# Kernel tuning notes

Measured on AMD Instinct MI355X. Metric: run time of the kernel, lower is better.

## Reference

```python
import jax, jax.numpy as jnp
import numpy as np
from jax import lax

EMB, HID, L, PATCH, IMG, K = 192, 64, 6, 4, 224, 8
FMAP = IMG // PATCH
N = FMAP * FMAP
B = 8
ALG = 4
GB_np = np.array([0, 1, 1, 2])  # grade of each blade [1, e1, e2, e12]
GB = jnp.asarray(GB_np)

def _cayley_np():
    C = np.zeros((4, 4, 4), np.float32)
    tbl = {(0,0):(0,1.),(0,1):(1,1.),(0,2):(2,1.),(0,3):(3,1.),
           (1,0):(1,1.),(1,1):(0,1.),(1,2):(3,1.),(1,3):(2,1.),
           (2,0):(2,1.),(2,1):(3,-1.),(2,2):(0,1.),(2,3):(1,-1.),
           (3,0):(3,1.),(3,1):(2,-1.),(3,2):(1,1.),(3,3):(0,-1.)}
    for (i, j), (k, s) in tbl.items():
        C[i, j, k] = s
    return C

CAY_np = _cayley_np()
CAYLEY = jnp.asarray(CAY_np)
_paths = np.zeros((3, 3, 3), bool)
for _i in range(4):
    for _j in range(4):
        for _k in range(4):
            if CAY_np[_i, _j, _k] != 0:
                _paths[GB_np[_i], GB_np[_j], GB_np[_k]] = True
PI, PJ, PK = (jnp.asarray(a) for a in np.nonzero(_paths))
NPATH = int(_paths.sum())  # 10 geometric-product paths for Cl(2,0)

def build_knn_graph(H, W, k):
    yy, xx = np.meshgrid(np.arange(H, dtype=np.float32), np.arange(W, dtype=np.float32), indexing='ij')
    coords = np.stack([xx.ravel(), yy.ravel()], -1)
    cn = coords / np.array([W - 1, H - 1], np.float32) * 2 - 1
    d = np.linalg.norm(cn[:, None] - cn[None], axis=-1)
    np.fill_diagonal(d, np.inf)
    idx = np.argsort(d, axis=-1, kind='stable')[:, :k]
    rows = np.repeat(np.arange(H * W), k)
    cols = idx.reshape(-1)
    return rows.astype(np.int32), cols.astype(np.int32), cn.astype(np.float32)

def mvlin(x, W, b=None):
    # per-grade MVLinear: W [out,in,3] expanded to blades via GB
    y = jnp.einsum('nmi,bmi->bni', W[:, :, GB], x)
    if b is not None:
        y = y.at[:, :, 0].add(b)  # bias embedded in scalar blade only
    return y

def mvlin_flat(x, W, b):
    # subspaces=False MVLinear: same weight across blades
    y = jnp.einsum('nm,bmi->bni', W, x)
    return y.at[:, :, 0].add(b)

def mv_silu(x, a, b):
    # invariants: [scalar, q(grade1), q(grade2)]; gate = sigmoid(a*inv+b)
    inv = jnp.concatenate([x[..., :1], x[..., 1:2]**2 + x[..., 2:3]**2, x[..., 3:4]**2], -1)
    return jax.nn.sigmoid(a * inv + b)[..., GB] * x

def normalize_mv(x, a):
    q = jnp.concatenate([x[..., :1]**2, x[..., 1:2]**2 + x[..., 2:3]**2, x[..., 3:4]**2], -1)
    n = jnp.sqrt(q + 1e-12)
    d = jax.nn.sigmoid(a) * (n - 1.0) + 1.0
    return x / (d + 1e-6)[..., GB]

def sgp(x, Wl, bl, Wr, na, gw):
    # SteerableGeometricProductLayer
    xr = normalize_mv(mvlin(x, Wr), na)
    full = jnp.zeros((gw.shape[0], 3, 3, 3), x.dtype).at[:, PI, PJ, PK].set(gw)
    fb = full[:, GB][:, :, GB][:, :, :, GB]  # [feat,4,4,4]
    gp = jnp.einsum('bni,nijk,bnk->bnj', x, CAYLEY[None] * fb, xr)
    return (mvlin(x, Wl, bl) + gp) * np.float32(1.0 / np.sqrt(2.0))

def _forward(x, conv_w, conv_b, stem_g, stem_b, pos_embed, in_W, in_b, in_Wl, in_bl, in_Wr, in_na, in_gw, eg_eW, eg_eb, eg_sa, eg_sb, eg_nW, eg_nb, eg_Wl, eg_bl, eg_Wr, eg_na, eg_gw, eg_aa, eg_ab, out_W, out_b, on_g, on_b, cls_W, cls_b, coords, rows, cols):
    Bx = x.shape[0]
    # stem: strided conv + LayerNorm over (C,H,W)
    y = lax.conv_general_dilated(x, conv_w, (PATCH, PATCH), 'VALID', dimension_numbers=('NCHW', 'OIHW', 'NCHW')) + conv_b[None, :, None, None]
    mu = y.mean(axis=(1, 2, 3), keepdims=True)
    var = ((y - mu) ** 2).mean(axis=(1, 2, 3), keepdims=True)
    y = (y - mu) / jnp.sqrt(var + 1e-5) * stem_g[None] + stem_b[None]
    y = y + pos_embed
    feat = y.transpose(0, 2, 3, 1).reshape(Bx * N, EMB)
    # embed features in scalar blade, coordinates in vector blades e1,e2
    h = jnp.zeros((Bx * N, EMB + 1, ALG), x.dtype)
    h = h.at[:, :EMB, 0].set(feat)
    h = h.at[:, EMB, 1:3].set(jnp.tile(coords, (Bx, 1)))
    h = sgp(mvlin_flat(h, in_W, in_b), in_Wl, in_bl, in_Wr, in_na, in_gw)
    BN = Bx * N
    for i in range(L):
        m = mv_silu(mvlin(h[rows] - h[cols], eg_eW[i], eg_eb[i]), eg_sa[i], eg_sb[i])
        agg = jax.ops.segment_sum(m, rows, num_segments=BN)  # count computed but unused in original
        nu = mvlin(jnp.concatenate([h, agg], axis=1), eg_nW[i], eg_nb[i])
        out = mv_silu(sgp(nu, eg_Wl[i], eg_bl[i], eg_Wr[i], eg_na[i], eg_gw[i]), eg_aa[i], eg_ab[i])
        h = h + out if i > 0 else out
    s = mvlin_flat(h, out_W, out_b)[..., 0]
    mu2 = s.mean(-1, keepdims=True)
    v2 = ((s - mu2) ** 2).mean(-1, keepdims=True)
    s = (s - mu2) / jnp.sqrt(v2 + 1e-5) * on_g + on_b
    pooled = s.reshape(Bx, N, EMB).mean(axis=1)
    return pooled @ cls_W.T + cls_b

def setup_inputs() -> dict:
    key = jax.random.key(0)
    ks = iter(jax.random.split(key, 64))
    nrm = lambda shape, s=0.05: jax.random.normal(next(ks), shape, jnp.float32) * s
    rows, cols, cn = build_knn_graph(FMAP, FMAP, K)
    offs = np.arange(B, dtype=np.int32)[:, None] * N
    rows_b = (rows[None] + offs).reshape(-1)
    cols_b = (cols[None] + offs).reshape(-1)
    return dict(
        x=jax.random.normal(next(ks), (B, 3, IMG, IMG), jnp.float32),
        conv_w=nrm((EMB, 3, PATCH, PATCH)),
        conv_b=jnp.zeros((EMB,), jnp.float32),
        stem_g=jnp.ones((EMB, FMAP, FMAP), jnp.float32),
        stem_b=jnp.zeros((EMB, FMAP, FMAP), jnp.float32),
        pos_embed=nrm((1, EMB, FMAP, FMAP), 0.02),
        coords=jnp.asarray(cn),
        in_W=nrm((HID, EMB + 1)), in_b=jnp.zeros((HID,), jnp.float32),
        in_Wl=nrm((HID, HID, 3)), in_bl=jnp.zeros((HID,), jnp.float32),
        in_Wr=nrm((HID, HID, 3)), in_na=jnp.zeros((HID, 3), jnp.float32),
        in_gw=nrm((HID, NPATH), 0.2),
        eg_eW=nrm((L, HID, HID, 3)), eg_eb=jnp.zeros((L, HID), jnp.float32),
        eg_sa=jnp.ones((L, HID, 3), jnp.float32), eg_sb=jnp.zeros((L, HID, 3), jnp.float32),
        eg_nW=nrm((L, HID, 2 * HID, 3)), eg_nb=jnp.zeros((L, HID), jnp.float32),
        eg_Wl=nrm((L, HID, HID, 3)), eg_bl=jnp.zeros((L, HID), jnp.float32),
        eg_Wr=nrm((L, HID, HID, 3)), eg_na=jnp.zeros((L, HID, 3), jnp.float32),
        eg_gw=nrm((L, HID, NPATH), 0.2),
        eg_aa=jnp.ones((L, HID, 3), jnp.float32), eg_ab=jnp.zeros((L, HID, 3), jnp.float32),
        out_W=nrm((EMB, HID)), out_b=jnp.zeros((EMB,), jnp.float32),
        on_g=jnp.ones((EMB,), jnp.float32), on_b=jnp.zeros((EMB,), jnp.float32),
        cls_W=nrm((10, EMB), 0.02), cls_b=jnp.zeros((10,), jnp.float32),
        rows=jnp.asarray(rows_b), cols=jnp.asarray(cols_b),
    )

def reference(x, conv_w, conv_b, stem_g, stem_b, pos_embed, coords, in_W, in_b, in_Wl, in_bl, in_Wr, in_na, in_gw, eg_eW, eg_eb, eg_sa, eg_sb, eg_nW, eg_nb, eg_Wl, eg_bl, eg_Wr, eg_na, eg_gw, eg_aa, eg_ab, out_W, out_b, on_g, on_b, cls_W, cls_b, rows, cols):
    return _forward(x, conv_w, conv_b, stem_g, stem_b, pos_embed, in_W, in_b, in_Wl, in_bl, in_Wr, in_na, in_gw, eg_eW, eg_eb, eg_sa, eg_sb, eg_nW, eg_nb, eg_Wl, eg_bl, eg_Wr, eg_na, eg_gw, eg_aa, eg_ab, out_W, out_b, on_g, on_b, cls_W, cls_b, coords, rows, cols)
```

## Files before the change

kernel.cpp:

```cpp
#include <hip/hip_runtime.h>
#include <hip/hip_bf16.h>
#include <math.h>

#define EMBC   192
#define NLAY   6
#define IMGC   224
#define FMAPC  56
#define NNODE  3136
#define NBATCH 8
#define BNODES 25088
#define KNNE   8
#define NT     64
#define RSQRT2 0.70710678118654752f

__device__ __forceinline__ float sigm(float x){ return 1.0f/(1.0f+__expf(-x)); }

__device__ __forceinline__ void stage_tile(float* xs, const float* __restrict__ g,
                                           int p0, int tid){
  for(int t = tid; t < NT*256; t += 256){
    int n = t >> 8, q = t & 255;
    int m = q >> 2, bi = q & 3;
    xs[(n<<8) + (((m + n) & 63)<<2) + bi] = g[((size_t)(p0+n)<<8) + q];
  }
}

__global__ void k_tr(const float* __restrict__ g, const float* __restrict__ sb,
                     const float* __restrict__ pe, float* __restrict__ g2,
                     float* __restrict__ pb2){
  int n = blockIdx.x; int c = threadIdx.x;
  g2[n*EMBC + c]  = g[c*NNODE + n];
  pb2[n*EMBC + c] = sb[c*NNODE + n] + pe[c*NNODE + n];
}

__global__ __launch_bounds__(256) void k_conv(const float* __restrict__ x,
    const float* __restrict__ cw, const float* __restrict__ cb,
    float* __restrict__ y0, float* __restrict__ parts){
  __shared__ float xs[2688];
  __shared__ float wsh[9216];
  __shared__ float red[512];
  int blk = blockIdx.x; int b = blk / FMAPC; int ph = blk % FMAPC;
  int tid = threadIdx.x;
  for(int t = tid; t < 9216; t += 256) wsh[t] = cw[t];
  for(int t = tid; t < 2688; t += 256){
    int r = t / IMGC; int w = t % IMGC;
    int ci = r >> 2, kh = r & 3;
    xs[t] = x[((size_t)(b*3 + ci)*IMGC + (ph*4 + kh))*IMGC + w];
  }
  __syncthreads();
  float s1 = 0.f, s2 = 0.f;
  for(int oi = tid; oi < FMAPC*EMBC; oi += 256){
    int pw = oi / EMBC; int c = oi % EMBC;
    float acc = cb[c];
    const float4* wv4 = (const float4*)(wsh + c*48);
    #pragma unroll
    for(int r = 0; r < 12; ++r){
      float4 xv = *((const float4*)(xs + r*IMGC + pw*4));
      float4 wv = wv4[r];
      acc += xv.x*wv.x + xv.y*wv.y + xv.z*wv.z + xv.w*wv.w;
    }
    y0[((size_t)(b*NNODE + ph*FMAPC + pw))*EMBC + c] = acc;
    s1 += acc; s2 += acc*acc;
  }
  red[tid] = s1; red[256+tid] = s2;
  __syncthreads();
  for(int st = 128; st > 0; st >>= 1){
    if(tid < st){ red[tid] += red[tid+st]; red[256+tid] += red[256+tid+st]; }
    __syncthreads();
  }
  if(tid == 0){ parts[blk*2] = red[0]; parts[blk*2+1] = red[256]; }
}

__global__ void k_stats(const float* __restrict__ parts, float* __restrict__ stats){
  int b = threadIdx.x;
  if(b < NBATCH){
    float S = 0.f, Q = 0.f;
    for(int j = 0; j < FMAPC; ++j){ S += parts[(b*FMAPC+j)*2]; Q += parts[(b*FMAPC+j)*2+1]; }
    float cnt = (float)(EMBC*NNODE);
    float mu = S/cnt;
    float var = Q/cnt - mu*mu;
    stats[b*2] = mu; stats[b*2+1] = rsqrtf(var + 1e-5f);
  }
}

__global__ __launch_bounds__(256,2) void k_embed(const float* __restrict__ y0,
    const float* __restrict__ stats, const float* __restrict__ g2,
    const float* __restrict__ pb2, const float* __restrict__ inW,
    const float* __restrict__ inb, const float* __restrict__ coords,
    float* __restrict__ xmv){
  __shared__ float fs[NT*193];
  int tid = threadIdx.x, lane = tid & 63;
  int wid = __builtin_amdgcn_readfirstlane(tid >> 6);
  int ch0 = wid << 4;
  int p0 = blockIdx.x * NT;
  int b = p0 / NNODE; int n0 = p0 - b*NNODE;
  float mu = stats[b*2], rstd = stats[b*2+1];
  for(int t = tid; t < NT*192; t += 256){
    int n = t / 192, c = t - n*192;
    int nn = n0 + n;
    fs[n*193 + c] = (y0[(size_t)(p0+n)*192 + c] - mu)*rstd*g2[nn*192+c] + pb2[nn*192+c];
  }
  __syncthreads();
  float acc[16];
  #pragma unroll
  for(int ci = 0; ci < 16; ++ci) acc[ci] = 0.f;
  for(int m = 0; m < 192; ++m){
    float xm = fs[lane*193 + m];
    #pragma unroll
    for(int ci = 0; ci < 16; ++ci)
      acc[ci] += inW[(size_t)(ch0+ci)*193 + m] * xm;
  }
  float cx = coords[(n0+lane)*2], cy = coords[(n0+lane)*2+1];
  #pragma unroll
  for(int ci = 0; ci < 16; ++ci){
    int ch = ch0 + ci;
    float wc = inW[(size_t)ch*193 + 192];
    float4 v; v.x = acc[ci] + inb[ch]; v.y = wc*cx; v.z = wc*cy; v.w = 0.f;
    *((float4*)(xmv + ((size_t)(p0+lane)*64 + ch)*4)) = v;
  }
}

__global__ __launch_bounds__(256) void k_edge(const float* __restrict__ z,
    const int* __restrict__ cols, const float* __restrict__ eb,
    const float* __restrict__ sa, const float* __restrict__ sb,
    float* __restrict__ agg){
  int tid = threadIdx.x;
  int ch = tid & 63;
  int p = blockIdx.x*4 + (tid >> 6);
  float4 zo = *((const float4*)(z + ((size_t)p*64 + ch)*4));
  float bias = eb[ch];
  float a0 = sa[ch*3], a1 = sa[ch*3+1], a2 = sa[ch*3+2];
  float b0 = sb[ch*3], b1 = sb[ch*3+1], b2 = sb[ch*3+2];
  float ax=0.f, ay=0.f, az=0.f, aw=0.f;
  #pragma unroll
  for(int k = 0; k < KNNE; ++k){
    int c = cols[p*KNNE + k];
    float4 zc = *((const float4*)(z + ((size_t)c*64 + ch)*4));
    float d0 = zo.x - zc.x + bias;
    float d1 = zo.y - zc.y;
    float d2 = zo.z - zc.z;
    float d3 = zo.w - zc.w;
    float g0 = sigm(a0*d0 + b0);
    float g1 = sigm(a1*(d1*d1 + d2*d2) + b1);
    float g2v = sigm(a2*(d3*d3) + b2);
    ax += g0*d0; ay += g1*d1; az += g1*d2; aw += g2v*d3;
  }
  float4 acc; acc.x=ax; acc.y=ay; acc.z=az; acc.w=aw;
  *((float4*)(agg + ((size_t)p*64 + ch)*4)) = acc;
}

__global__ __launch_bounds__(256,2) void k_nu(const float* __restrict__ h,
    const float* __restrict__ agg, float* __restrict__ nu,
    const float* __restrict__ W, const float* __restrict__ nb){
  __shared__ float xs[NT*256];
  int tid = threadIdx.x, lane = tid & 63;
  int wid = __builtin_amdgcn_readfirstlane(tid >> 6);
  int ch0 = wid << 4;
  int p0 = blockIdx.x * NT;
  float acc[16][4];
  #pragma unroll
  for(int ci = 0; ci < 16; ++ci)
    #pragma unroll
    for(int bi = 0; bi < 4; ++bi) acc[ci][bi] = 0.f;
  const float* xbase = xs + (lane<<8);

  stage_tile(xs, h, p0, tid);
  __syncthreads();
  #pragma unroll 1
  for(int m = 0; m < 64; ++m){
    float4 xv = *((const float4*)(xbase + (((m + lane)&63)<<2)));
    #pragma unroll
    for(int ci = 0; ci < 16; ++ci){
      const float* wp = W + ((size_t)(ch0+ci)*128 + m)*3;
      float w0 = wp[0], w1 = wp[1], w2 = wp[2];
      acc[ci][0] += w0*xv.x; acc[ci][1] += w1*xv.y;
      acc[ci][2] += w1*xv.z; acc[ci][3] += w2*xv.w;
    }
  }
  __syncthreads();
  stage_tile(xs, agg, p0, tid);
  __syncthreads();
  #pragma unroll 1
  for(int m = 0; m < 64; ++m){
    float4 xv = *((const float4*)(xbase + (((m + lane)&63)<<2)));
    #pragma unroll
    for(int ci = 0; ci < 16; ++ci){
      const float* wp = W + ((size_t)(ch0+ci)*128 + 64 + m)*3;
      float w0 = wp[0], w1 = wp[1], w2 = wp[2];
      acc[ci][0] += w0*xv.x; acc[ci][1] += w1*xv.y;
      acc[ci][2] += w1*xv.z; acc[ci][3] += w2*xv.w;
    }
  }
  int p = p0 + lane;
  #pragma unroll
  for(int ci = 0; ci < 16; ++ci){
    int ch = ch0 + ci;
    float4 v; v.x = acc[ci][0] + nb[ch]; v.y = acc[ci][1];
    v.z = acc[ci][2]; v.w = acc[ci][3];
    *((float4*)(nu + ((size_t)p*64 + ch)*4)) = v;
  }
}

__global__ __launch_bounds__(256,2) void k_sgp(const float* __restrict__ src,
    float* __restrict__ h, const float* __restrict__ Wl, const float* __restrict__ bl,
    const float* __restrict__ Wr, const float* __restrict__ na,
    const float* __restrict__ gw, const float* __restrict__ aa,
    const float* __restrict__ ab, int mode,
    const float* __restrict__ zW, float* __restrict__ zout){
  __shared__ float xs[NT*256];
  int tid = threadIdx.x, lane = tid & 63;
  int wid = __builtin_amdgcn_readfirstlane(tid >> 6);
  int ch0 = wid << 4;
  int p0 = blockIdx.x * NT;
  stage_tile(xs, src, p0, tid);
  __syncthreads();
  float accl[16][4], accr[16][4];
  #pragma unroll
  for(int ci = 0; ci < 16; ++ci)
    #pragma unroll
    for(int bi = 0; bi < 4; ++bi){ accl[ci][bi] = 0.f; accr[ci][bi] = 0.f; }
  const float* xbase = xs + (lane<<8);
  #pragma unroll 1
  for(int m = 0; m < 64; ++m){
    float4 xv = *((const float4*)(xbase + (((m + lane)&63)<<2)));
    #pragma unroll
    for(int ci = 0; ci < 16; ++ci){
      const float* wlp = Wl + ((size_t)(ch0+ci)*64 + m)*3;
      const float* wrp = Wr + ((size_t)(ch0+ci)*64 + m)*3;
      float wl0 = wlp[0], wl1 = wlp[1], wl2 = wlp[2];
      float wr0 = wrp[0], wr1 = wrp[1], wr2 = wrp[2];
      accl[ci][0] += wl0*xv.x; accl[ci][1] += wl1*xv.y;
      accl[ci][2] += wl1*xv.z; accl[ci][3] += wl2*xv.w;
      accr[ci][0] += wr0*xv.x; accr[ci][1] += wr1*xv.y;
      accr[ci][2] += wr1*xv.z; accr[ci][3] += wr2*xv.w;
    }
  }
  float vout[16][4];
  int p = p0 + lane;
  #pragma unroll
  for(int ci = 0; ci < 16; ++ci){
    int ch = ch0 + ci;
    float yr0 = accr[ci][0], yr1 = accr[ci][1], yr2 = accr[ci][2], yr3 = accr[ci][3];
    float na0 = sigm(na[ch*3]), na1 = sigm(na[ch*3+1]), na2 = sigm(na[ch*3+2]);
    float d0 = na0*(sqrtf(yr0*yr0 + 1e-12f) - 1.f) + 1.f + 1e-6f;
    float d1 = na1*(sqrtf(yr1*yr1 + yr2*yr2 + 1e-12f) - 1.f) + 1.f + 1e-6f;
    float d2 = na2*(sqrtf(yr3*yr3 + 1e-12f) - 1.f) + 1.f + 1e-6f;
    float xr0 = yr0/d0, xr1 = yr1/d1, xr2 = yr2/d1, xr3 = yr3/d2;
    float4 xv = *((const float4*)(xbase + (((ch + lane)&63)<<2)));
    const float* gwp = gw + ch*10;
    float gp0 = gwp[0]*xv.x*xr0 + gwp[3]*(xv.y*xr1 + xv.z*xr2) + gwp[7]*xv.w*xr3;
    float gp1 = gwp[1]*xv.x*xr1 + gwp[4]*xv.y*xr0 - gwp[5]*xv.z*xr3 - gwp[8]*xv.w*xr2;
    float gp2 = gwp[1]*xv.x*xr2 + gwp[4]*xv.z*xr0 + gwp[5]*xv.y*xr3 + gwp[8]*xv.w*xr1;
    float gp3 = gwp[2]*xv.x*xr3 + gwp[6]*(xv.y*xr2 - xv.z*xr1) - gwp[9]*xv.w*xr0;
    float o0 = (accl[ci][0] + bl[ch] + gp0)*RSQRT2;
    float o1 = (accl[ci][1] + gp1)*RSQRT2;
    float o2 = (accl[ci][2] + gp2)*RSQRT2;
    float o3 = (accl[ci][3] + gp3)*RSQRT2;
    float v0, v1, v2, v3;
    if(mode == 0){ v0 = o0; v1 = o1; v2 = o2; v3 = o3; }
    else{
      float g0 = sigm(aa[ch*3]*o0 + ab[ch*3]);
      float g1 = sigm(aa[ch*3+1]*(o1*o1 + o2*o2) + ab[ch*3+1]);
      float g2v = sigm(aa[ch*3+2]*(o3*o3) + ab[ch*3+2]);
      v0 = g0*o0; v1 = g1*o1; v2 = g1*o2; v3 = g2v*o3;
      if(mode == 2){
        float4 hp = *((const float4*)(h + ((size_t)p*64 + ch)*4));
        v0 += hp.x; v1 += hp.y; v2 += hp.z; v3 += hp.w;
      }
    }
    float4 vv; vv.x=v0; vv.y=v1; vv.z=v2; vv.w=v3;
    *((float4*)(h + ((size_t)p*64 + ch)*4)) = vv;
    vout[ci][0]=v0; vout[ci][1]=v1; vout[ci][2]=v2; vout[ci][3]=v3;
  }
  if(zW != nullptr){
    __syncthreads();
    #pragma unroll
    for(int ci = 0; ci < 16; ++ci){
      int ch = ch0 + ci;
      float4 vv; vv.x=vout[ci][0]; vv.y=vout[ci][1]; vv.z=vout[ci][2]; vv.w=vout[ci][3];
      *((float4*)(xs + (lane<<8) + (((ch + lane)&63)<<2))) = vv;
    }
    __syncthreads();
    float accz[16][4];
    #pragma unroll
    for(int ci = 0; ci < 16; ++ci)
      #pragma unroll
      for(int bi = 0; bi < 4; ++bi) accz[ci][bi] = 0.f;
    #pragma unroll 1
    for(int m = 0; m < 64; ++m){
      float4 xv = *((const float4*)(xbase + (((m + lane)&63)<<2)));
      #pragma unroll
      for(int ci = 0; ci < 16; ++ci){
        const float* wp = zW + ((size_t)(ch0+ci)*64 + m)*3;
        float w0 = wp[0], w1 = wp[1], w2 = wp[2];
        accz[ci][0] += w0*xv.x; accz[ci][1] += w1*xv.y;
        accz[ci][2] += w1*xv.z; accz[ci][3] += w2*xv.w;
      }
    }
    #pragma unroll
    for(int ci = 0; ci < 16; ++ci){
      int ch = ch0 + ci;
      float4 v; v.x=accz[ci][0]; v.y=accz[ci][1]; v.z=accz[ci][2]; v.w=accz[ci][3];
      *((float4*)(zout + ((size_t)p*64 + ch)*4)) = v;
    }
  }
}

__global__ __launch_bounds__(256,2) void k_head(const float* __restrict__ h,
    const float* __restrict__ oW, const float* __restrict__ ob,
    const float* __restrict__ ong, const float* __restrict__ onb,
    float* __restrict__ s){
  __shared__ float hs[NT*65];
  __shared__ float rr[512];
  int tid = threadIdx.x, lane = tid & 63;
  int wid = __builtin_amdgcn_readfirstlane(tid >> 6);
  int c0 = wid*48;
  int p0 = blockIdx.x * NT;
  for(int t = tid; t < NT*64; t += 256){
    int n = t >> 6, c = t & 63;
    hs[n*65 + c] = h[(((size_t)(p0+n))*64 + c)*4];
  }
  __syncthreads();
  float a[48];
  #pragma unroll
  for(int ci = 0; ci < 48; ++ci) a[ci] = 0.f;
  #pragma unroll 1
  for(int m = 0; m < 64; ++m){
    float xm = hs[lane*65 + m];
    #pragma unroll
    for(int ci = 0; ci < 48; ++ci)
      a[ci] += oW[(size_t)(c0+ci)*64 + m] * xm;
  }
  float s1 = 0.f, s2 = 0.f;
  #pragma unroll
  for(int ci = 0; ci < 48; ++ci){
    a[ci] += ob[c0+ci];
    s1 += a[ci]; s2 += a[ci]*a[ci];
  }
  rr[wid*64 + lane] = s1; rr[256 + wid*64 + lane] = s2;
  __syncthreads();
  float S = rr[lane] + rr[64+lane] + rr[128+lane] + rr[192+lane];
  float Q = rr[256+lane] + rr[320+lane] + rr[384+lane] + rr[448+lane];
  float mu = S*(1.0f/EMBC);
  float var = Q*(1.0f/EMBC) - mu*mu;
  float rstd = rsqrtf(var + 1e-5f);
  #pragma unroll
  for(int q = 0; q < 12; ++q){
    int c = c0 + q*4;
    float4 v;
    v.x = (a[q*4  ] - mu)*rstd*ong[c  ] + onb[c  ];
    v.y = (a[q*4+1] - mu)*rstd*ong[c+1] + onb[c+1];
    v.z = (a[q*4+2] - mu)*rstd*ong[c+2] + onb[c+2];
    v.w = (a[q*4+3] - mu)*rstd*ong[c+3] + onb[c+3];
    *((float4*)(s + (size_t)(p0+lane)*192 + c)) = v;
  }
}

__global__ void k_pool1(const float* __restrict__ s, float* __restrict__ pp){
  int blk = blockIdx.x;
  int b = blk >> 5, chunk = blk & 31;
  int c = threadIdx.x;
  float acc = 0.f;
  int n0 = chunk*98;
  for(int j = 0; j < 98; ++j) acc += s[((size_t)(b*NNODE + n0 + j))*EMBC + c];
  pp[(size_t)blk*EMBC + c] = acc;
}
__global__ void k_pool2(const float* __restrict__ pp, float* __restrict__ pooled){
  int b = blockIdx.x; int c = threadIdx.x;
  float acc = 0.f;
  for(int j = 0; j < 32; ++j) acc += pp[((size_t)(b*32 + j))*EMBC + c];
  pooled[b*EMBC + c] = acc * (1.0f/NNODE);
}

__global__ void k_cls(const float* __restrict__ pooled, const float* __restrict__ cW,
                      const float* __restrict__ cb, float* __restrict__ out){
  int tid = threadIdx.x;
  if(tid < NBATCH*10){
    int b = tid/10, k = tid%10;
    float acc = cb[k];
    for(int c = 0; c < EMBC; ++c) acc += pooled[b*EMBC + c]*cW[k*EMBC + c];
    out[tid] = acc;
  }
}

extern "C" void kernel_launch(void* const* d_in, const int* in_sizes, int n_in,
                              void* d_out, int out_size, void* d_ws, size_t ws_size,
                              hipStream_t stream){
  const float* x      = (const float*)d_in[0];
  const float* conv_w = (const float*)d_in[1];
  const float* conv_b = (const float*)d_in[2];
  const float* stem_g = (const float*)d_in[3];
  const float* stem_b = (const float*)d_in[4];
  const float* pos_e  = (const float*)d_in[5];
  const float* coords = (const float*)d_in[6];
  const float* inW    = (const float*)d_in[7];
  const float* inb    = (const float*)d_in[8];
  const float* inWl   = (const float*)d_in[9];
  const float* inbl   = (const float*)d_in[10];
  const float* inWr   = (const float*)d_in[11];
  const float* inna   = (const float*)d_in[12];
  const float* ingw   = (const float*)d_in[13];
  const float* eg_eW  = (const float*)d_in[14];
  const float* eg_eb  = (const float*)d_in[15];
  const float* eg_sa  = (const float*)d_in[16];
  const float* eg_sb  = (const float*)d_in[17];
  const float* eg_nW  = (const float*)d_in[18];
  const float* eg_nb  = (const float*)d_in[19];
  const float* eg_Wl  = (const float*)d_in[20];
  const float* eg_bl  = (const float*)d_in[21];
  const float* eg_Wr  = (const float*)d_in[22];
  const float* eg_na  = (const float*)d_in[23];
  const float* eg_gw  = (const float*)d_in[24];
  const float* eg_aa  = (const float*)d_in[25];
  const float* eg_ab  = (const float*)d_in[26];
  const float* outW   = (const float*)d_in[27];
  const float* outb   = (const float*)d_in[28];
  const float* ong    = (const float*)d_in[29];
  const float* onb    = (const float*)d_in[30];
  const float* clsW   = (const float*)d_in[31];
  const float* clsb   = (const float*)d_in[32];
  const int*   cols   = (const int*)d_in[34];

  float* ws = (float*)d_ws;
  size_t off = 0;
  float* hbuf  = ws + off; off += (size_t)BNODES*256;
  float* bigA  = ws + off; off += (size_t)BNODES*256;
  float* bigB  = ws + off; off += (size_t)BNODES*256;
  float* g2    = ws + off; off += (size_t)NNODE*EMBC;
  float* pb2   = ws + off; off += (size_t)NNODE*EMBC;
  float* y0    = ws + off; off += (size_t)BNODES*EMBC;
  float* parts = ws + off; off += 896;
  float* stats = ws + off; off += 16;
  float* pp    = ws + off; off += 256*EMBC;
  float* pooled= ws + off; off += NBATCH*EMBC;

  const int NTILE = BNODES/NT;

  k_tr   <<<NNODE, 192, 0, stream>>>(stem_g, stem_b, pos_e, g2, pb2);
  k_conv <<<NBATCH*FMAPC, 256, 0, stream>>>(x, conv_w, conv_b, y0, parts);
  k_stats<<<1, 64, 0, stream>>>(parts, stats);
  k_embed<<<NTILE, 256, 0, stream>>>(y0, stats, g2, pb2, inW, inb, coords, bigA);
  k_sgp  <<<NTILE, 256, 0, stream>>>(bigA, hbuf, inWl, inbl, inWr, inna, ingw,
                                     (const float*)nullptr, (const float*)nullptr, 0,
                                     eg_eW, bigB);
  float* zcur = bigB;
  float* spare = bigA;
  for(int l = 0; l < NLAY; ++l){
    k_edge <<<BNODES/4, 256, 0, stream>>>(zcur, cols, eg_eb + l*64,
                                          eg_sa + l*192, eg_sb + l*192, spare);
    k_nu   <<<NTILE, 256, 0, stream>>>(hbuf, spare, zcur,
                                       eg_nW + (size_t)l*24576, eg_nb + l*64);
    const float* zWn = (l < NLAY-1) ? (eg_eW + (size_t)(l+1)*12288) : (const float*)nullptr;
    k_sgp  <<<NTILE, 256, 0, stream>>>(zcur, hbuf, eg_Wl + (size_t)l*12288, eg_bl + l*64,
                                       eg_Wr + (size_t)l*12288, eg_na + l*192,
                                       eg_gw + l*640, eg_aa + l*192, eg_ab + l*192,
                                       (l==0)?1:2, zWn, spare);
    float* t = zcur; zcur = spare; spare = t;
  }
  k_head <<<NTILE, 256, 0, stream>>>(hbuf, outW, outb, ong, onb, spare);
  k_pool1<<<256, 192, 0, stream>>>(spare, pp);
  k_pool2<<<8, 192, 0, stream>>>(pp, pooled);
  k_cls  <<<1, 128, 0, stream>>>(pooled, clsW, clsb, (float*)d_out);
}
```

Baseline: 1.342 ms.

## Fuse edge, node-update and SGP into one per-layer kernel with repacked weights

Merges the edge aggregation, node-update linear and steerable geometric product stages of each layer into a single 512-thread kernel. Aggregated messages and the node-update output now pass through shared memory instead of global buffers. Weights are transposed once into m-major layouts so each wave reads contiguous channel weights. Global stores are coalesced through an LDS copy-out, and the y0 buffer is aliased onto bigB. The costs are repack launches on every call and heavier per-block work with more synchronisation, while doing the edge gather inside the fused kernel may hurt latency hiding.

Result: slower. 1.793 ms (+33.6%).

```diff
diff --git a/kernel.cpp b/kernel.cpp
--- a/kernel.cpp
+++ b/kernel.cpp
@@ -15,12 +15,22 @@
 
 __device__ __forceinline__ float sigm(float x){ return 1.0f/(1.0f+__expf(-x)); }
 
-__device__ __forceinline__ void stage_tile(float* xs, const float* __restrict__ g,
-                                           int p0, int tid){
-  for(int t = tid; t < NT*256; t += 256){
-    int n = t >> 8, q = t & 255;
-    int m = q >> 2, bi = q & 3;
-    xs[(n<<8) + (((m + n) & 63)<<2) + bi] = g[((size_t)(p0+n)<<8) + q];
+__global__ void k_repack3(const float* __restrict__ src, float* __restrict__ dst, int K){
+  int l = blockIdx.y;
+  size_t S = (size_t)64*K*3;
+  int t = blockIdx.x*256 + threadIdx.x;
+  if(t < (int)S){
+    int j = t % 3; int r = t / 3;
+    int m = r % K, ch = r / K;
+    dst[l*S + ((size_t)m*64 + ch)*3 + j] = src[l*S + ((size_t)ch*K + m)*3 + j];
+  }
+}
+__global__ void k_repack1(const float* __restrict__ src, float* __restrict__ dst,
+                          int R, int K){
+  int t = blockIdx.x*256 + threadIdx.x;
+  if(t < R*K){
+    int m = t % K, r = t / K;
+    dst[m*R + r] = src[r*K + m];
   }
 }
 
@@ -84,7 +94,7 @@
 
 __global__ __launch_bounds__(256,2) void k_embed(const float* __restrict__ y0,
     const float* __restrict__ stats, const float* __restrict__ g2,
-    const float* __restrict__ pb2, const float* __restrict__ inW,
+    const float* __restrict__ pb2, const float* __restrict__ inWp,
     const float* __restrict__ inb, const float* __restrict__ coords,
     float* __restrict__ xmv){
   __shared__ float fs[NT*193];
@@ -103,141 +113,242 @@
   float acc[16];
   #pragma unroll
   for(int ci = 0; ci < 16; ++ci) acc[ci] = 0.f;
+  #pragma unroll 2
   for(int m = 0; m < 192; ++m){
     float xm = fs[lane*193 + m];
-    #pragma unroll
-    for(int ci = 0; ci < 16; ++ci)
-      acc[ci] += inW[(size_t)(ch0+ci)*193 + m] * xm;
+    const float* wp = inWp + m*64 + ch0;
+    #pragma unroll
+    for(int ci = 0; ci < 16; ++ci) acc[ci] += wp[ci]*xm;
   }
   float cx = coords[(n0+lane)*2], cy = coords[(n0+lane)*2+1];
   #pragma unroll
   for(int ci = 0; ci < 16; ++ci){
     int ch = ch0 + ci;
-    float wc = inW[(size_t)ch*193 + 192];
+    float wc = inWp[192*64 + ch];
     float4 v; v.x = acc[ci] + inb[ch]; v.y = wc*cx; v.z = wc*cy; v.w = 0.f;
     *((float4*)(xmv + ((size_t)(p0+lane)*64 + ch)*4)) = v;
   }
 }
 
-__global__ __launch_bounds__(256) void k_edge(const float* __restrict__ z,
-    const int* __restrict__ cols, const float* __restrict__ eb,
-    const float* __restrict__ sa, const float* __restrict__ sb,
-    float* __restrict__ agg){
-  int tid = threadIdx.x;
-  int ch = tid & 63;
-  int p = blockIdx.x*4 + (tid >> 6);
-  float4 zo = *((const float4*)(z + ((size_t)p*64 + ch)*4));
-  float bias = eb[ch];
-  float a0 = sa[ch*3], a1 = sa[ch*3+1], a2 = sa[ch*3+2];
-  float b0 = sb[ch*3], b1 = sb[ch*3+1], b2 = sb[ch*3+2];
-  float ax=0.f, ay=0.f, az=0.f, aw=0.f;
-  #pragma unroll
-  for(int k = 0; k < KNNE; ++k){
-    int c = cols[p*KNNE + k];
-    float4 zc = *((const float4*)(z + ((size_t)c*64 + ch)*4));
-    float d0 = zo.x - zc.x + bias;
-    float d1 = zo.y - zc.y;
-    float d2 = zo.z - zc.z;
-    float d3 = zo.w - zc.w;
-    float g0 = sigm(a0*d0 + b0);
-    float g1 = sigm(a1*(d1*d1 + d2*d2) + b1);
-    float g2v = sigm(a2*(d3*d3) + b2);
-    ax += g0*d0; ay += g1*d1; az += g1*d2; aw += g2v*d3;
-  }
-  float4 acc; acc.x=ax; acc.y=ay; acc.z=az; acc.w=aw;
-  *((float4*)(agg + ((size_t)p*64 + ch)*4)) = acc;
-}
-
-__global__ __launch_bounds__(256,2) void k_nu(const float* __restrict__ h,
-    const float* __restrict__ agg, float* __restrict__ nu,
-    const float* __restrict__ W, const float* __restrict__ nb){
+__device__ __forceinline__ void stage512(float* xs, const float* __restrict__ g,
+                                         int p0, int tid){
+  for(int t = tid; t < NT*256; t += 512){
+    int n = t >> 8, q = t & 255;
+    int m = q >> 2, bi = q & 3;
+    xs[(n<<8) + (((m + n) & 63)<<2) + bi] = g[((size_t)(p0+n)<<8) + q];
+  }
+}
+__device__ __forceinline__ void copyout512(const float* xs, float* __restrict__ g,
+                                           int p0, int tid){
+  for(int t = tid; t < NT*64; t += 512){
+    int n = t >> 6, mq = t & 63;
+    float4 v = *((const float4*)(xs + (n<<8) + (((mq + n)&63)<<2)));
+    *((float4*)(g + ((size_t)(p0+n)<<8) + (mq<<2))) = v;
+  }
+}
+
+__global__ __launch_bounds__(512,2) void k_sgp0(const float* __restrict__ src,
+    float* __restrict__ h, float* __restrict__ zout,
+    const float* __restrict__ Wlp, const float* __restrict__ bl,
+    const float* __restrict__ Wrp, const float* __restrict__ na,
+    const float* __restrict__ gw, const float* __restrict__ zWp){
   __shared__ float xs[NT*256];
   int tid = threadIdx.x, lane = tid & 63;
   int wid = __builtin_amdgcn_readfirstlane(tid >> 6);
-  int ch0 = wid << 4;
+  int ch0 = wid << 3;
   int p0 = blockIdx.x * NT;
-  float acc[16][4];
-  #pragma unroll
-  for(int ci = 0; ci < 16; ++ci)
-    #pragma unroll
-    for(int bi = 0; bi < 4; ++bi) acc[ci][bi] = 0.f;
+  stage512(xs, src, p0, tid);
+  __syncthreads();
   const float* xbase = xs + (lane<<8);
-
-  stage_tile(xs, h, p0, tid);
-  __syncthreads();
+  float accl[8][4], accr[8][4];
+  #pragma unroll
+  for(int ci = 0; ci < 8; ++ci)
+    #pragma unroll
+    for(int bi = 0; bi < 4; ++bi){ accl[ci][bi]=0.f; accr[ci][bi]=0.f; }
   #pragma unroll 1
   for(int m = 0; m < 64; ++m){
     float4 xv = *((const float4*)(xbase + (((m + lane)&63)<<2)));
-    #pragma unroll
-    for(int ci = 0; ci < 16; ++ci){
-      const float* wp = W + ((size_t)(ch0+ci)*128 + m)*3;
-      float w0 = wp[0], w1 = wp[1], w2 = wp[2];
-      acc[ci][0] += w0*xv.x; acc[ci][1] += w1*xv.y;
-      acc[ci][2] += w1*xv.z; acc[ci][3] += w2*xv.w;
-    }
-  }
-  __syncthreads();
-  stage_tile(xs, agg, p0, tid);
-  __syncthreads();
-  #pragma unroll 1
-  for(int m = 0; m < 64; ++m){
-    float4 xv = *((const float4*)(xbase + (((m + lane)&63)<<2)));
-    #pragma unroll
-    for(int ci = 0; ci < 16; ++ci){
-      const float* wp = W + ((size_t)(ch0+ci)*128 + 64 + m)*3;
-      float w0 = wp[0], w1 = wp[1], w2 = wp[2];
-      acc[ci][0] += w0*xv.x; acc[ci][1] += w1*xv.y;
-      acc[ci][2] += w1*xv.z; acc[ci][3] += w2*xv.w;
-    }
-  }
-  int p = p0 + lane;
-  #pragma unroll
-  for(int ci = 0; ci < 16; ++ci){
-    int ch = ch0 + ci;
-    float4 v; v.x = acc[ci][0] + nb[ch]; v.y = acc[ci][1];
-    v.z = acc[ci][2]; v.w = acc[ci][3];
-    *((float4*)(nu + ((size_t)p*64 + ch)*4)) = v;
-  }
-}
-
-__global__ __launch_bounds__(256,2) void k_sgp(const float* __restrict__ src,
-    float* __restrict__ h, const float* __restrict__ Wl, const float* __restrict__ bl,
-    const float* __restrict__ Wr, const float* __restrict__ na,
-    const float* __restrict__ gw, const float* __restrict__ aa,
-    const float* __restrict__ ab, int mode,
-    const float* __restrict__ zW, float* __restrict__ zout){
-  __shared__ float xs[NT*256];
-  int tid = threadIdx.x, lane = tid & 63;
-  int wid = __builtin_amdgcn_readfirstlane(tid >> 6);
-  int ch0 = wid << 4;
-  int p0 = blockIdx.x * NT;
-  stage_tile(xs, src, p0, tid);
-  __syncthreads();
-  float accl[16][4], accr[16][4];
-  #pragma unroll
-  for(int ci = 0; ci < 16; ++ci)
-    #pragma unroll
-    for(int bi = 0; bi < 4; ++bi){ accl[ci][bi] = 0.f; accr[ci][bi] = 0.f; }
-  const float* xbase = xs + (lane<<8);
-  #pragma unroll 1
-  for(int m = 0; m < 64; ++m){
-    float4 xv = *((const float4*)(xbase + (((m + lane)&63)<<2)));
-    #pragma unroll
-    for(int ci = 0; ci < 16; ++ci){
-      const float* wlp = Wl + ((size_t)(ch0+ci)*64 + m)*3;
-      const float* wrp = Wr + ((size_t)(ch0+ci)*64 + m)*3;
-      float wl0 = wlp[0], wl1 = wlp[1], wl2 = wlp[2];
-      float wr0 = wrp[0], wr1 = wrp[1], wr2 = wrp[2];
+    const float* wlp = Wlp + ((size_t)m*64 + ch0)*3;
+    const float* wrp = Wrp + ((size_t)m*64 + ch0)*3;
+    #pragma unroll
+    for(int ci = 0; ci < 8; ++ci){
+      float wl0 = wlp[ci*3], wl1 = wlp[ci*3+1], wl2 = wlp[ci*3+2];
+      float wr0 = wrp[ci*3], wr1 = wrp[ci*3+1], wr2 = wrp[ci*3+2];
       accl[ci][0] += wl0*xv.x; accl[ci][1] += wl1*xv.y;
       accl[ci][2] += wl1*xv.z; accl[ci][3] += wl2*xv.w;
       accr[ci][0] += wr0*xv.x; accr[ci][1] += wr1*xv.y;
       accr[ci][2] += wr1*xv.z; accr[ci][3] += wr2*xv.w;
     }
   }
-  float vout[16][4];
+  #pragma unroll
+  for(int ci = 0; ci < 8; ++ci){
+    int ch = ch0 + ci;
+    float yr0 = accr[ci][0], yr1 = accr[ci][1], yr2 = accr[ci][2], yr3 = accr[ci][3];
+    float na0 = sigm(na[ch*3]), na1 = sigm(na[ch*3+1]), na2 = sigm(na[ch*3+2]);
+    float d0 = na0*(sqrtf(yr0*yr0 + 1e-12f) - 1.f) + 1.f + 1e-6f;
+    float d1 = na1*(sqrtf(yr1*yr1 + yr2*yr2 + 1e-12f) - 1.f) + 1.f + 1e-6f;
+    float d2 = na2*(sqrtf(yr3*yr3 + 1e-12f) - 1.f) + 1.f + 1e-6f;
+    float xr0 = yr0/d0, xr1 = yr1/d1, xr2 = yr2/d1, xr3 = yr3/d2;
+    float4 xv = *((const float4*)(xbase + (((ch + lane)&63)<<2)));
+    const float* gwp = gw + ch*10;
+    float gp0 = gwp[0]*xv.x*xr0 + gwp[3]*(xv.y*xr1 + xv.z*xr2) + gwp[7]*xv.w*xr3;
+    float gp1 = gwp[1]*xv.x*xr1 + gwp[4]*xv.y*xr0 - gwp[5]*xv.z*xr3 - gwp[8]*xv.w*xr2;
+    float gp2 = gwp[1]*xv.x*xr2 + gwp[4]*xv.z*xr0 + gwp[5]*xv.y*xr3 + gwp[8]*xv.w*xr1;
+    float gp3 = gwp[2]*xv.x*xr3 + gwp[6]*(xv.y*xr2 - xv.z*xr1) - gwp[9]*xv.w*xr0;
+    accl[ci][0] = (accl[ci][0] + bl[ch] + gp0)*RSQRT2;
+    accl[ci][1] = (accl[ci][1] + gp1)*RSQRT2;
+    accl[ci][2] = (accl[ci][2] + gp2)*RSQRT2;
+    accl[ci][3] = (accl[ci][3] + gp3)*RSQRT2;
+  }
+  __syncthreads();
+  #pragma unroll
+  for(int ci = 0; ci < 8; ++ci){
+    int ch = ch0 + ci;
+    float4 v; v.x=accl[ci][0]; v.y=accl[ci][1]; v.z=accl[ci][2]; v.w=accl[ci][3];
+    *((float4*)(xs + (lane<<8) + (((ch + lane)&63)<<2))) = v;
+  }
+  __syncthreads();
+  copyout512(xs, h, p0, tid);
+  float az[8][4];
+  #pragma unroll
+  for(int ci = 0; ci < 8; ++ci)
+    #pragma unroll
+    for(int bi = 0; bi < 4; ++bi) az[ci][bi] = 0.f;
+  #pragma unroll 1
+  for(int m = 0; m < 64; ++m){
+    float4 xv = *((const float4*)(xbase + (((m + lane)&63)<<2)));
+    const float* wp = zWp + ((size_t)m*64 + ch0)*3;
+    #pragma unroll
+    for(int ci = 0; ci < 8; ++ci){
+      float w0 = wp[ci*3], w1 = wp[ci*3+1], w2 = wp[ci*3+2];
+      az[ci][0] += w0*xv.x; az[ci][1] += w1*xv.y;
+      az[ci][2] += w1*xv.z; az[ci][3] += w2*xv.w;
+    }
+  }
+  __syncthreads();
+  #pragma unroll
+  for(int ci = 0; ci < 8; ++ci){
+    int ch = ch0 + ci;
+    float4 v; v.x=az[ci][0]; v.y=az[ci][1]; v.z=az[ci][2]; v.w=az[ci][3];
+    *((float4*)(xs + (lane<<8) + (((ch + lane)&63)<<2))) = v;
+  }
+  __syncthreads();
+  copyout512(xs, zout, p0, tid);
+}
+
+__global__ __launch_bounds__(512,2) void k_layer(
+    float* __restrict__ h, const float* __restrict__ z,
+    float* __restrict__ zout, const int* __restrict__ cols,
+    const float* __restrict__ eb, const float* __restrict__ sa,
+    const float* __restrict__ sb,
+    const float* __restrict__ nWp, const float* __restrict__ nb,
+    const float* __restrict__ Wlp, const float* __restrict__ bl,
+    const float* __restrict__ Wrp, const float* __restrict__ na,
+    const float* __restrict__ gw, const float* __restrict__ aa,
+    const float* __restrict__ ab,
+    const float* __restrict__ zWp, int mode){
+  __shared__ float xs[NT*256];
+  int tid = threadIdx.x, lane = tid & 63;
+  int wid = __builtin_amdgcn_readfirstlane(tid >> 6);
+  int p0 = blockIdx.x * NT;
+  float ag[8][4];
+  {
+    int ch = lane;
+    float ebv = eb[ch];
+    float a0 = sa[ch*3], a1 = sa[ch*3+1], a2 = sa[ch*3+2];
+    float b0 = sb[ch*3], b1 = sb[ch*3+1], b2 = sb[ch*3+2];
+    #pragma unroll
+    for(int e = 0; e < 8; ++e){
+      int p = p0 + wid*8 + e;
+      float4 zo = *((const float4*)(z + ((size_t)p*64 + ch)*4));
+      float ax=0.f, ay=0.f, az_=0.f, aw=0.f;
+      #pragma unroll
+      for(int k = 0; k < KNNE; ++k){
+        int c = cols[p*KNNE + k];
+        float4 zc = *((const float4*)(z + ((size_t)c*64 + ch)*4));
+        float d0 = zo.x - zc.x + ebv;
+        float d1 = zo.y - zc.y;
+        float d2 = zo.z - zc.z;
+        float d3 = zo.w - zc.w;
+        float g0 = sigm(a0*d0 + b0);
+        float g1 = sigm(a1*(d1*d1 + d2*d2) + b1);
+        float g2v = sigm(a2*(d3*d3) + b2);
+        ax += g0*d0; ay += g1*d1; az_ += g1*d2; aw += g2v*d3;
+      }
+      ag[e][0]=ax; ag[e][1]=ay; ag[e][2]=az_; ag[e][3]=aw;
+    }
+  }
+  stage512(xs, h, p0, tid);
+  __syncthreads();
+  int ch0 = wid << 3;
+  const float* xbase = xs + (lane<<8);
+  float acc[8][4];
+  #pragma unroll
+  for(int ci = 0; ci < 8; ++ci)
+    #pragma unroll
+    for(int bi = 0; bi < 4; ++bi) acc[ci][bi] = 0.f;
+  #pragma unroll 1
+  for(int m = 0; m < 64; ++m){
+    float4 xv = *((const float4*)(xbase + (((m + lane)&63)<<2)));
+    const float* wp = nWp + ((size_t)m*64 + ch0)*3;
+    #pragma unroll
+    for(int ci = 0; ci < 8; ++ci){
+      float w0 = wp[ci*3], w1 = wp[ci*3+1], w2 = wp[ci*3+2];
+      acc[ci][0] += w0*xv.x; acc[ci][1] += w1*xv.y;
+      acc[ci][2] += w1*xv.z; acc[ci][3] += w2*xv.w;
+    }
+  }
+  __syncthreads();
+  #pragma unroll
+  for(int e = 0; e < 8; ++e){
+    int n = wid*8 + e;
+    float4 v; v.x=ag[e][0]; v.y=ag[e][1]; v.z=ag[e][2]; v.w=ag[e][3];
+    *((float4*)(xs + (n<<8) + (((lane + n)&63)<<2))) = v;
+  }
+  __syncthreads();
+  #pragma unroll 1
+  for(int m = 0; m < 64; ++m){
+    float4 xv = *((const float4*)(xbase + (((m + lane)&63)<<2)));
+    const float* wp = nWp + ((size_t)(64+m)*64 + ch0)*3;
+    #pragma unroll
+    for(int ci = 0; ci < 8; ++ci){
+      float w0 = wp[ci*3], w1 = wp[ci*3+1], w2 = wp[ci*3+2];
+      acc[ci][0] += w0*xv.x; acc[ci][1] += w1*xv.y;
+      acc[ci][2] += w1*xv.z; acc[ci][3] += w2*xv.w;
+    }
+  }
+  __syncthreads();
+  #pragma unroll
+  for(int ci = 0; ci < 8; ++ci){
+    int ch = ch0 + ci;
+    float4 v; v.x = acc[ci][0] + nb[ch]; v.y = acc[ci][1];
+    v.z = acc[ci][2]; v.w = acc[ci][3];
+    *((float4*)(xs + (lane<<8) + (((ch + lane)&63)<<2))) = v;
+  }
+  __syncthreads();
+  float accl[8][4], accr[8][4];
+  #pragma unroll
+  for(int ci = 0; ci < 8; ++ci)
+    #pragma unroll
+    for(int bi = 0; bi < 4; ++bi){ accl[ci][bi]=0.f; accr[ci][bi]=0.f; }
+  #pragma unroll 1
+  for(int m = 0; m < 64; ++m){
+    float4 xv = *((const float4*)(xbase + (((m + lane)&63)<<2)));
+    const float* wlp = Wlp + ((size_t)m*64 + ch0)*3;
+    const float* wrp = Wrp + ((size_t)m*64 + ch0)*3;
+    #pragma unroll
+    for(int ci = 0; ci < 8; ++ci){
+      float wl0 = wlp[ci*3], wl1 = wlp[ci*3+1], wl2 = wlp[ci*3+2];
+      float wr0 = wrp[ci*3], wr1 = wrp[ci*3+1], wr2 = wrp[ci*3+2];
+      accl[ci][0] += wl0*xv.x; accl[ci][1] += wl1*xv.y;
+      accl[ci][2] += wl1*xv.z; accl[ci][3] += wl2*xv.w;
+      accr[ci][0] += wr0*xv.x; accr[ci][1] += wr1*xv.y;
+      accr[ci][2] += wr1*xv.z; accr[ci][3] += wr2*xv.w;
+    }
+  }
   int p = p0 + lane;
   #pragma unroll
-  for(int ci = 0; ci < 16; ++ci){
+  for(int ci = 0; ci < 8; ++ci){
     int ch = ch0 + ci;
     float yr0 = accr[ci][0], yr1 = accr[ci][1], yr2 = accr[ci][2], yr3 = accr[ci][3];
     float na0 = sigm(na[ch*3]), na1 = sigm(na[ch*3+1]), na2 = sigm(na[ch*3+2]);
@@ -255,58 +366,56 @@
     float o1 = (accl[ci][1] + gp1)*RSQRT2;
     float o2 = (accl[ci][2] + gp2)*RSQRT2;
     float o3 = (accl[ci][3] + gp3)*RSQRT2;
-    float v0, v1, v2, v3;
-    if(mode == 0){ v0 = o0; v1 = o1; v2 = o2; v3 = o3; }
-    else{
-      float g0 = sigm(aa[ch*3]*o0 + ab[ch*3]);
-      float g1 = sigm(aa[ch*3+1]*(o1*o1 + o2*o2) + ab[ch*3+1]);
-      float g2v = sigm(aa[ch*3+2]*(o3*o3) + ab[ch*3+2]);
-      v0 = g0*o0; v1 = g1*o1; v2 = g1*o2; v3 = g2v*o3;
-      if(mode == 2){
-        float4 hp = *((const float4*)(h + ((size_t)p*64 + ch)*4));
-        v0 += hp.x; v1 += hp.y; v2 += hp.z; v3 += hp.w;
-      }
-    }
-    float4 vv; vv.x=v0; vv.y=v1; vv.z=v2; vv.w=v3;
-    *((float4*)(h + ((size_t)p*64 + ch)*4)) = vv;
-    vout[ci][0]=v0; vout[ci][1]=v1; vout[ci][2]=v2; vout[ci][3]=v3;
-  }
-  if(zW != nullptr){
-    __syncthreads();
-    #pragma unroll
-    for(int ci = 0; ci < 16; ++ci){
-      int ch = ch0 + ci;
-      float4 vv; vv.x=vout[ci][0]; vv.y=vout[ci][1]; vv.z=vout[ci][2]; vv.w=vout[ci][3];
-      *((float4*)(xs + (lane<<8) + (((ch + lane)&63)<<2))) = vv;
-    }
-    __syncthreads();
-    float accz[16][4];
-    #pragma unroll
-    for(int ci = 0; ci < 16; ++ci)
+    float g0 = sigm(aa[ch*3]*o0 + ab[ch*3]);
+    float g1 = sigm(aa[ch*3+1]*(o1*o1 + o2*o2) + ab[ch*3+1]);
+    float g2v = sigm(aa[ch*3+2]*(o3*o3) + ab[ch*3+2]);
+    float v0 = g0*o0, v1 = g1*o1, v2 = g1*o2, v3 = g2v*o3;
+    if(mode == 2){
+      float4 hp = *((const float4*)(h + ((size_t)p*64 + ch)*4));
+      v0 += hp.x; v1 += hp.y; v2 += hp.z; v3 += hp.w;
+    }
+    accl[ci][0]=v0; accl[ci][1]=v1; accl[ci][2]=v2; accl[ci][3]=v3;
+  }
+  __syncthreads();
+  #pragma unroll
+  for(int ci = 0; ci < 8; ++ci){
+    int ch = ch0 + ci;
+    float4 v; v.x=accl[ci][0]; v.y=accl[ci][1]; v.z=accl[ci][2]; v.w=accl[ci][3];
+    *((float4*)(xs + (lane<<8) + (((ch + lane)&63)<<2))) = v;
+  }
+  __syncthreads();
+  copyout512(xs, h, p0, tid);
+  if(zWp != nullptr){
+    float az[8][4];
+    #pragma unroll
+    for(int ci = 0; ci < 8; ++ci)
       #pragma unroll
-      for(int bi = 0; bi < 4; ++bi) accz[ci][bi] = 0.f;
+      for(int bi = 0; bi < 4; ++bi) az[ci][bi] = 0.f;
     #pragma unroll 1
     for(int m = 0; m < 64; ++m){
       float4 xv = *((const float4*)(xbase + (((m + lane)&63)<<2)));
+      const float* wp = zWp + ((size_t)m*64 + ch0)*3;
       #pragma unroll
-      for(int ci = 0; ci < 16; ++ci){
-        const float* wp = zW + ((size_t)(ch0+ci)*64 + m)*3;
-        float w0 = wp[0], w1 = wp[1], w2 = wp[2];
-        accz[ci][0] += w0*xv.x; accz[ci][1] += w1*xv.y;
-        accz[ci][2] += w1*xv.z; accz[ci][3] += w2*xv.w;
+      for(int ci = 0; ci < 8; ++ci){
+        float w0 = wp[ci*3], w1 = wp[ci*3+1], w2 = wp[ci*3+2];
+        az[ci][0] += w0*xv.x; az[ci][1] += w1*xv.y;
+        az[ci][2] += w1*xv.z; az[ci][3] += w2*xv.w;
       }
     }
-    #pragma unroll
-    for(int ci = 0; ci < 16; ++ci){
+    __syncthreads();
+    #pragma unroll
+    for(int ci = 0; ci < 8; ++ci){
       int ch = ch0 + ci;
-      float4 v; v.x=accz[ci][0]; v.y=accz[ci][1]; v.z=accz[ci][2]; v.w=accz[ci][3];
-      *((float4*)(zout + ((size_t)p*64 + ch)*4)) = v;
-    }
+      float4 v; v.x=az[ci][0]; v.y=az[ci][1]; v.z=az[ci][2]; v.w=az[ci][3];
+      *((float4*)(xs + (lane<<8) + (((ch + lane)&63)<<2))) = v;
+    }
+    __syncthreads();
+    copyout512(xs, zout, p0, tid);
   }
 }
 
 __global__ __launch_bounds__(256,2) void k_head(const float* __restrict__ h,
-    const float* __restrict__ oW, const float* __restrict__ ob,
+    const float* __restrict__ oWp, const float* __restrict__ ob,
     const float* __restrict__ ong, const float* __restrict__ onb,
     float* __restrict__ s){
   __shared__ float hs[NT*65];
@@ -326,9 +435,9 @@
   #pragma unroll 1
   for(int m = 0; m < 64; ++m){
     float xm = hs[lane*65 + m];
-    #pragma unroll
-    for(int ci = 0; ci < 48; ++ci)
-      a[ci] += oW[(size_t)(c0+ci)*64 + m] * xm;
+    const float* wp = oWp + m*192 + c0;
+    #pragma unroll
+    for(int ci = 0; ci < 48; ++ci) a[ci] += wp[ci]*xm;
   }
   float s1 = 0.f, s2 = 0.f;
   #pragma unroll
@@ -427,36 +536,51 @@
   float* bigB  = ws + off; off += (size_t)BNODES*256;
   float* g2    = ws + off; off += (size_t)NNODE*EMBC;
   float* pb2   = ws + off; off += (size_t)NNODE*EMBC;
-  float* y0    = ws + off; off += (size_t)BNODES*EMBC;
   float* parts = ws + off; off += 896;
   float* stats = ws + off; off += 16;
   float* pp    = ws + off; off += 256*EMBC;
   float* pooled= ws + off; off += NBATCH*EMBC;
+  float* wpInW = ws + off; off += 193*64;
+  float* wpOW  = ws + off; off += 64*192;
+  float* wpInWl= ws + off; off += 12288;
+  float* wpInWr= ws + off; off += 12288;
+  float* wpEW  = ws + off; off += (size_t)NLAY*12288;
+  float* wpWl  = ws + off; off += (size_t)NLAY*12288;
+  float* wpWr  = ws + off; off += (size_t)NLAY*12288;
+  float* wpNW  = ws + off; off += (size_t)NLAY*24576;
+  float* y0    = bigB;
 
   const int NTILE = BNODES/NT;
+
+  { dim3 g1((12352+255)/256); k_repack1<<<g1, 256, 0, stream>>>(inW,  wpInW, 64, 193); }
+  { dim3 g1((12288+255)/256); k_repack1<<<g1, 256, 0, stream>>>(outW, wpOW, 192, 64); }
+  { dim3 g3((12288+255)/256, 1); k_repack3<<<g3, 256, 0, stream>>>(inWl, wpInWl, 64); }
+  { dim3 g3((12288+255)/256, 1); k_repack3<<<g3, 256, 0, stream>>>(inWr, wpInWr, 64); }
+  { dim3 g3((12288+255)/256, NLAY); k_repack3<<<g3, 256, 0, stream>>>(eg_eW, wpEW, 64); }
+  { dim3 g3((12288+255)/256, NLAY); k_repack3<<<g3, 256, 0, stream>>>(eg_Wl, wpWl, 64); }
+  { dim3 g3((12288+255)/256, NLAY); k_repack3<<<g3, 256, 0, stream>>>(eg_Wr, wpWr, 64); }
+  { dim3 g3((24576+255)/256, NLAY); k_repack3<<<g3, 256, 0, stream>>>(eg_nW, wpNW, 128); }
 
   k_tr   <<<NNODE, 192, 0, stream>>>(stem_g, stem_b, pos_e, g2, pb2);
   k_conv <<<NBATCH*FMAPC, 256, 0, stream>>>(x, conv_w, conv_b, y0, parts);
   k_stats<<<1, 64, 0, stream>>>(parts, stats);
-  k_embed<<<NTILE, 256, 0, stream>>>(y0, stats, g2, pb2, inW, inb, coords, bigA);
-  k_sgp  <<<NTILE, 256, 0, stream>>>(bigA, hbuf, inWl, inbl, inWr, inna, ingw,
-                                     (const float*)nullptr, (const float*)nullptr, 0,
-                                     eg_eW, bigB);
+  k_embed<<<NTILE, 256, 0, stream>>>(y0, stats, g2, pb2, wpInW, inb, coords, bigA);
+  k_sgp0 <<<NTILE, 512, 0, stream>>>(bigA, hbuf, bigB, wpInWl, inbl, wpInWr,
+                                     inna, ingw, wpEW);
   float* zcur = bigB;
   float* spare = bigA;
   for(int l = 0; l < NLAY; ++l){
-    k_edge <<<BNODES/4, 256, 0, stream>>>(zcur, cols, eg_eb + l*64,
-                                          eg_sa + l*192, eg_sb + l*192, spare);
-    k_nu   <<<NTILE, 256, 0, stream>>>(hbuf, spare, zcur,
-                                       eg_nW + (size_t)l*24576, eg_nb + l*64);
-    const float* zWn = (l < NLAY-1) ? (eg_eW + (size_t)(l+1)*12288) : (const float*)nullptr;
-    k_sgp  <<<NTILE, 256, 0, stream>>>(zcur, hbuf, eg_Wl + (size_t)l*12288, eg_bl + l*64,
-                                       eg_Wr + (size_t)l*12288, eg_na + l*192,
-                                       eg_gw + l*640, eg_aa + l*192, eg_ab + l*192,
-                                       (l==0)?1:2, zWn, spare);
-    float* t = zcur; zcur = spare; spare = t;
-  }
-  k_head <<<NTILE, 256, 0, stream>>>(hbuf, outW, outb, ong, onb, spare);
+    const float* zWn = (l < NLAY-1) ? (wpEW + (size_t)(l+1)*12288) : (const float*)nullptr;
+    k_layer<<<NTILE, 512, 0, stream>>>(hbuf, zcur, spare, cols,
+        eg_eb + l*64, eg_sa + l*192, eg_sb + l*192,
+        wpNW + (size_t)l*24576, eg_nb + l*64,
+        wpWl + (size_t)l*12288, eg_bl + l*64,
+        wpWr + (size_t)l*12288, eg_na + l*192,
+        eg_gw + l*640, eg_aa + l*192, eg_ab + l*192,
+        zWn, (l==0)?1:2);
+    if(l < NLAY-1){ float* t = zcur; zcur = spare; spare = t; }
+  }
+  k_head <<<NTILE, 256, 0, stream>>>(hbuf, wpOW, outb, ong, onb, spare);
   k_pool1<<<256, 192, 0, stream>>>(spare, pp);
   k_pool2<<<8, 192, 0, stream>>>(pp, pooled);
   k_cls  <<<1, 128, 0, stream>>>(pooled, clsW, clsb, (float*)d_out);
```
